# Kernel optimization log

Hardware: AMD Instinct MI355X
Metric: run time of the kernel (lower is better)

Reference implementation:

```python
import jax, jax.numpy as jnp
import numpy as np

N = 50000      # num_nodes
E = 800000     # undirected edge count (maps holds 2E directed maps)
D = 4          # stalk dimension


def setup_inputs() -> dict:
    key = jax.random.key(0)
    k1, k2, k3 = jax.random.split(key, 3)
    maps = jax.random.normal(k1, (2 * E, D, D), dtype=jnp.float32) * 0.3
    # ensure every node appears as a source at least once (avoids degenerate
    # identity eigenproblems for isolated nodes)
    row = jnp.concatenate([jnp.arange(N, dtype=jnp.int32),
                           jax.random.randint(k2, (E - N,), 0, N, dtype=jnp.int32)])
    col = jax.random.randint(k3, (E,), 0, N, dtype=jnp.int32)
    # second half of edge_index is the reversed orientation, as the module assumes
    edge_index = jnp.stack([jnp.concatenate([row, col]),
                            jnp.concatenate([col, row])])
    return {"maps": maps, "edge_index": edge_index, "num_nodes": N}


def reference(maps, edge_index, num_nodes):
    n = num_nodes
    d = maps.shape[1]
    twoE = maps.shape[0]
    Ee = twoE // 2
    row_all = edge_index[0]                                   # [2E]
    # diag contribution: R^T R per directed edge, scatter-added onto source node
    diag_contrib = jnp.einsum('eki,ekj->eij', maps, maps)     # [2E,d,d]
    maps_diag = jnp.zeros((n, d, d), maps.dtype).at[row_all].add(diag_contrib)
    row = edge_index[0, :Ee]
    col = edge_index[1, :Ee]
    # off-diagonal block: R_ij^T R_ji per undirected edge
    maps_triu = jnp.einsum('eki,ekj->eij', maps[:Ee], maps[Ee:])  # [E,d,d]
    # eval-mode augmentation: + I
    to_inv = maps_diag + jnp.eye(d, dtype=maps.dtype)
    evals, evecs = jnp.linalg.eigh(to_inv)                    # batched tiny eigh
    inv_sqrt = jnp.einsum('nik,nk,njk->nij', evecs,
                          jnp.clip(evals, 1e-8, None) ** -0.5, evecs)
    # normalize: D^{-1/2} blocks, clamp to [-1, 1]
    maps_triu = jnp.clip(jnp.einsum('eik,ekl,elj->eij',
                                    inv_sqrt[row], maps_triu, inv_sqrt[col]), -1.0, 1.0)
    maps_diag = jnp.clip(jnp.einsum('nik,nkl,nlj->nij',
                                    inv_sqrt, maps_diag, inv_sqrt), -1.0, 1.0)
    # COO assembly of the (n*d, n*d) sheaf Laplacian
    ar = jnp.arange(d, dtype=jnp.int32)
    A, B = jnp.meshgrid(ar, ar, indexing='ij')                # [d,d]
    node = jnp.arange(n, dtype=jnp.int32)
    diag_rows = (node[:, None, None] * d + A).reshape(-1)
    diag_cols = (node[:, None, None] * d + B).reshape(-1)
    tri_rows_ij = (row[:, None, None] * d + A).reshape(-1)
    tri_cols_ij = (col[:, None, None] * d + B).reshape(-1)
    tri_rows_ji = (col[:, None, None] * d + A).reshape(-1)
    tri_cols_ji = (row[:, None, None] * d + B).reshape(-1)
    rows = jnp.concatenate([diag_rows, tri_rows_ij, tri_rows_ji])
    cols = jnp.concatenate([diag_cols, tri_cols_ij, tri_cols_ji])
    vals = jnp.concatenate([maps_diag.reshape(-1),
                            (-maps_triu).reshape(-1),
                            (-jnp.swapaxes(maps_triu, 1, 2)).reshape(-1)])
    indices = jnp.stack([rows, cols])                         # [2, K]
    return indices, vals
```

## Files before the change

### kernel.cpp

```cpp
#include <hip/hip_runtime.h>

#define DEG_CAP 96

__device__ __forceinline__ void load4x4(const float* __restrict__ p, float m[4][4]) {
    const float4* q = (const float4*)p;
#pragma unroll
    for (int k = 0; k < 4; ++k) {
        float4 v = q[k];
        m[k][0] = v.x; m[k][1] = v.y; m[k][2] = v.z; m[k][3] = v.w;
    }
}

__device__ __forceinline__ void store4x4(float* __restrict__ p, const float m[4][4]) {
    float4* q = (float4*)p;
#pragma unroll
    for (int k = 0; k < 4; ++k)
        q[k] = make_float4(m[k][0], m[k][1], m[k][2], m[k][3]);
}

__device__ __forceinline__ void mmTa(const float a[4][4], const float b[4][4], float o[4][4]) {
#pragma unroll
    for (int i = 0; i < 4; ++i)
#pragma unroll
        for (int j = 0; j < 4; ++j)
            o[i][j] = a[0][i]*b[0][j] + a[1][i]*b[1][j] + a[2][i]*b[2][j] + a[3][i]*b[3][j];
}

__device__ __forceinline__ void mm(const float a[4][4], const float b[4][4], float o[4][4]) {
#pragma unroll
    for (int i = 0; i < 4; ++i)
#pragma unroll
        for (int j = 0; j < 4; ++j)
            o[i][j] = a[i][0]*b[0][j] + a[i][1]*b[1][j] + a[i][2]*b[2][j] + a[i][3]*b[3][j];
}

__global__ void k_fill(const int* __restrict__ ei, int* __restrict__ cnt,
                       int* __restrict__ bucket, int twoE) {
    int e = blockIdx.x * blockDim.x + threadIdx.x;
    if (e >= twoE) return;
    int node = ei[e];
    int slot = atomicAdd(&cnt[(size_t)node * 16], 1);
    if (slot < DEG_CAP)
        bucket[(size_t)node * DEG_CAP + slot] = e;
}

__global__ void k_gather_wave(const float* __restrict__ maps, const int* __restrict__ cnt,
                              const int* __restrict__ bucket, float* __restrict__ gram,
                              int N) {
    int tid = blockIdx.x * blockDim.x + threadIdx.x;
    int n = tid >> 6;
    int lane = threadIdx.x & 63;
    if (n >= N) return;
    int d = cnt[(size_t)n * 16];
    if (d > DEG_CAP) d = DEG_CAP;

    float G[10];
#pragma unroll
    for (int t = 0; t < 10; ++t) G[t] = 0.0f;

#pragma unroll
    for (int rep = 0; rep < 2; ++rep) {
        int slot = lane + rep * 64;
        if (slot < d) {
            int e = bucket[(size_t)n * DEG_CAP + slot];
            float m[4][4];
            load4x4(maps + (size_t)e * 16, m);
            int t = 0;
#pragma unroll
            for (int i = 0; i < 4; ++i)
#pragma unroll
                for (int j = i; j < 4; ++j, ++t)
                    G[t] += m[0][i]*m[0][j] + m[1][i]*m[1][j] + m[2][i]*m[2][j] + m[3][i]*m[3][j];
        }
    }
#pragma unroll
    for (int msk = 1; msk < 64; msk <<= 1) {
#pragma unroll
        for (int t = 0; t < 10; ++t)
            G[t] += __shfl_xor(G[t], msk, 64);
    }
    if (lane == 0) {
        float* g = gram + (size_t)n * 16;
        *(float4*)(g)     = make_float4(G[0], G[1], G[2], G[3]);
        *(float4*)(g + 4) = make_float4(G[4], G[5], G[6], G[7]);
        *(float2*)(g + 8) = make_float2(G[8], G[9]);
    }
}

__global__ void k_diag(const float* __restrict__ gram, float* __restrict__ Rtab,
                       float* __restrict__ out_vals, int N) {
    int n = blockIdx.x * blockDim.x + threadIdx.x;
    if (n >= N) return;
    const float* g = gram + (size_t)n * 16;
    float G[10];
#pragma unroll
    for (int t = 0; t < 10; ++t) G[t] = g[t];
    float D[4][4];
    {
        int t = 0;
#pragma unroll
        for (int i = 0; i < 4; ++i)
#pragma unroll
            for (int j = i; j < 4; ++j, ++t) { D[i][j] = G[t]; D[j][i] = G[t]; }
    }
    float A[4][4], V[4][4];
#pragma unroll
    for (int i = 0; i < 4; ++i)
#pragma unroll
        for (int j = 0; j < 4; ++j) {
            A[i][j] = D[i][j] + (i == j ? 1.0f : 0.0f);
            V[i][j] = (i == j) ? 1.0f : 0.0f;
        }
    const int PP[6] = {0,0,0,1,1,2};
    const int QQ[6] = {1,2,3,2,3,3};
    for (int sweep = 0; sweep < 6; ++sweep) {
        for (int r = 0; r < 6; ++r) {
            int p = PP[r], q = QQ[r];
            float apq = A[p][q];
            if (fabsf(apq) < 1e-12f) continue;
            float tau = (A[q][q] - A[p][p]) / (2.0f * apq);
            float t = copysignf(1.0f, tau) / (fabsf(tau) + sqrtf(1.0f + tau * tau));
            float c = 1.0f / sqrtf(1.0f + t * t);
            float s = t * c;
#pragma unroll
            for (int k = 0; k < 4; ++k) {
                float akp = A[k][p], akq = A[k][q];
                A[k][p] = c * akp - s * akq;
                A[k][q] = s * akp + c * akq;
            }
#pragma unroll
            for (int k = 0; k < 4; ++k) {
                float apk = A[p][k], aqk = A[q][k];
                A[p][k] = c * apk - s * aqk;
                A[q][k] = s * apk + c * aqk;
            }
#pragma unroll
            for (int k = 0; k < 4; ++k) {
                float vkp = V[k][p], vkq = V[k][q];
                V[k][p] = c * vkp - s * vkq;
                V[k][q] = s * vkp + c * vkq;
            }
        }
    }
    float w[4];
#pragma unroll
    for (int k = 0; k < 4; ++k)
        w[k] = 1.0f / sqrtf(fmaxf(A[k][k], 1e-8f));
    float R[4][4];
#pragma unroll
    for (int i = 0; i < 4; ++i)
#pragma unroll
        for (int j = 0; j < 4; ++j)
            R[i][j] = V[i][0]*w[0]*V[j][0] + V[i][1]*w[1]*V[j][1]
                    + V[i][2]*w[2]*V[j][2] + V[i][3]*w[3]*V[j][3];
    store4x4(Rtab + (size_t)n * 16, R);
    float U[4][4], O[4][4];
    mm(R, D, U);
    mm(U, R, O);
#pragma unroll
    for (int i = 0; i < 4; ++i)
#pragma unroll
        for (int j = 0; j < 4; ++j)
            O[i][j] = fminf(fmaxf(O[i][j], -1.0f), 1.0f);
    store4x4(out_vals + (size_t)n * 16, O);
}

__global__ void k_edge(const float* __restrict__ maps, const int* __restrict__ ei,
                       const float* __restrict__ Rtab,
                       float* __restrict__ out, size_t Tot, int N, int E) {
    int e = blockIdx.x * blockDim.x + threadIdx.x;
    if (e >= E) return;
    float M1[4][4], M2[4][4];
    load4x4(maps + (size_t)e * 16, M1);
    load4x4(maps + (size_t)(E + e) * 16, M2);
    int r = ei[e];
    int c = ei[2 * E + e];
    float T[4][4];
    mmTa(M1, M2, T);
    float Rr[4][4], Rc[4][4];
    load4x4(Rtab + (size_t)r * 16, Rr);
    load4x4(Rtab + (size_t)c * 16, Rc);
    float U[4][4], S[4][4];
    mm(Rr, T, U);
    mm(U, Rc, S);
#pragma unroll
    for (int i = 0; i < 4; ++i)
#pragma unroll
        for (int j = 0; j < 4; ++j)
            S[i][j] = fminf(fmaxf(S[i][j], -1.0f), 1.0f);

    float* out_rows = out;
    float* out_cols = out + Tot;
    float* out_vals = out + 2 * Tot;

    float rb = (float)(r * 4);
    float cb = (float)(c * 4);

    {
        size_t base = (size_t)16 * N + (size_t)e * 16;
        float4* qr = (float4*)(out_rows + base);
        float4* qc = (float4*)(out_cols + base);
        float4* qv = (float4*)(out_vals + base);
#pragma unroll
        for (int i = 0; i < 4; ++i) {
            float ri = rb + (float)i;
            qr[i] = make_float4(ri, ri, ri, ri);
            qc[i] = make_float4(cb, cb + 1.0f, cb + 2.0f, cb + 3.0f);
            qv[i] = make_float4(-S[i][0], -S[i][1], -S[i][2], -S[i][3]);
        }
    }
    {
        size_t base = (size_t)16 * (N + (size_t)E) + (size_t)e * 16;
        float4* qr = (float4*)(out_rows + base);
        float4* qc = (float4*)(out_cols + base);
        float4* qv = (float4*)(out_vals + base);
#pragma unroll
        for (int i = 0; i < 4; ++i) {
            float ci = cb + (float)i;
            qr[i] = make_float4(ci, ci, ci, ci);
            qc[i] = make_float4(rb, rb + 1.0f, rb + 2.0f, rb + 3.0f);
            qv[i] = make_float4(-S[0][i], -S[1][i], -S[2][i], -S[3][i]);
        }
    }
}

__global__ void k_nodeB(float* __restrict__ out, size_t Tot, int N) {
    int n = blockIdx.x * blockDim.x + threadIdx.x;
    if (n >= N) return;
    float nb = (float)(n * 4);
    float4* qr = (float4*)(out + (size_t)n * 16);
    float4* qc = (float4*)(out + Tot + (size_t)n * 16);
#pragma unroll
    for (int i = 0; i < 4; ++i) {
        float ni = nb + (float)i;
        qr[i] = make_float4(ni, ni, ni, ni);
        qc[i] = make_float4(nb, nb + 1.0f, nb + 2.0f, nb + 3.0f);
    }
}

extern "C" void kernel_launch(void* const* d_in, const int* in_sizes, int n_in,
                              void* d_out, int out_size, void* d_ws, size_t ws_size,
                              hipStream_t stream) {
    const float* maps = (const float*)d_in[0];
    const int* ei = (const int*)d_in[1];

    int twoE = in_sizes[0] / 16;
    int E = twoE / 2;
    size_t Tot = (size_t)out_size / 3;
    int N = (int)(Tot / 16) - twoE;

    float* out = (float*)d_out;
    float* out_vals = out + 2 * Tot;

    int* bucket = (int*)(out + ((size_t)out_size - (size_t)DEG_CAP * N));
    int* cnt    = (int*)(out + ((size_t)out_size - (size_t)DEG_CAP * N - (size_t)N * 16));
    float* gram =        out + ((size_t)out_size - (size_t)DEG_CAP * N - (size_t)N * 32);
    float* Rtab = out;

    hipMemsetAsync(cnt, 0, (size_t)N * 16 * sizeof(int), stream);

    int bs = 256;
    k_fill<<<(twoE + bs - 1) / bs, bs, 0, stream>>>(ei, cnt, bucket, twoE);
    k_gather_wave<<<((size_t)N * 64 + bs - 1) / bs, bs, 0, stream>>>(maps, cnt, bucket, gram, N);
    k_diag<<<(N + bs - 1) / bs, bs, 0, stream>>>(gram, Rtab, out_vals, N);
    k_edge<<<(E + bs - 1) / bs, bs, 0, stream>>>(maps, ei, Rtab, out, Tot, N, E);
    k_nodeB<<<(N + bs - 1) / bs, bs, 0, stream>>>(out, Tot, N);
}
```

Baseline: 638.0 us.

## Shard per-node atomic counters, prefetch maps in fill, use nontemporal output stores

Per-node edge counters are split into four shards chosen by the edge index, each on its own cache line, so fewer atomics contend for the same address. The fill kernel also touches the first element of each maps row to warm the cache before the gather kernel reads it. All outputs from the edge and node kernels are now written with nontemporal stores, keeping the large streaming output from evicting useful cache lines. The trade-offs are a larger counter array to clear, an extra read in fill, and a per-shard cap of 32 that can drop edges for nodes whose degree is unevenly spread across shards.

After: 949.7 us. +48.9%, slower.

```diff
diff --git a/kernel.cpp b/kernel.cpp
--- a/kernel.cpp
+++ b/kernel.cpp
@@ -1,6 +1,15 @@
 #include <hip/hip_runtime.h>
 
-#define DEG_CAP 96
+#define DEG_CAP   128
+#define NSHARD    4
+#define SHARD_CAP 32
+
+typedef float f32x4 __attribute__((ext_vector_type(4)));
+
+__device__ __forceinline__ void store_nt4(float* p, float a, float b, float c, float d) {
+    f32x4 v = {a, b, c, d};
+    __builtin_nontemporal_store(v, (f32x4*)p);
+}
 
 __device__ __forceinline__ void load4x4(const float* __restrict__ p, float m[4][4]) {
     const float4* q = (const float4*)p;
@@ -34,14 +43,17 @@
             o[i][j] = a[i][0]*b[0][j] + a[i][1]*b[1][j] + a[i][2]*b[2][j] + a[i][3]*b[3][j];
 }
 
-__global__ void k_fill(const int* __restrict__ ei, int* __restrict__ cnt,
-                       int* __restrict__ bucket, int twoE) {
+__global__ void k_fill(const int* __restrict__ ei, const float* __restrict__ maps,
+                       int* __restrict__ cnt, int* __restrict__ bucket, int twoE) {
     int e = blockIdx.x * blockDim.x + threadIdx.x;
     if (e >= twoE) return;
+    float warm = maps[(size_t)e * 16];
+    asm volatile("" :: "v"(warm));
     int node = ei[e];
-    int slot = atomicAdd(&cnt[(size_t)node * 16], 1);
-    if (slot < DEG_CAP)
-        bucket[(size_t)node * DEG_CAP + slot] = e;
+    int shard = e & (NSHARD - 1);
+    int slot = atomicAdd(&cnt[(size_t)node * 64 + shard * 16], 1);
+    if (slot < SHARD_CAP)
+        bucket[(size_t)node * DEG_CAP + shard * SHARD_CAP + slot] = e;
 }
 
 __global__ void k_gather_wave(const float* __restrict__ maps, const int* __restrict__ cnt,
@@ -51,8 +63,13 @@
     int n = tid >> 6;
     int lane = threadIdx.x & 63;
     if (n >= N) return;
-    int d = cnt[(size_t)n * 16];
-    if (d > DEG_CAP) d = DEG_CAP;
+
+    int ds[NSHARD];
+#pragma unroll
+    for (int s = 0; s < NSHARD; ++s) {
+        int c = cnt[(size_t)n * 64 + s * 16];
+        ds[s] = c > SHARD_CAP ? SHARD_CAP : c;
+    }
 
     float G[10];
 #pragma unroll
@@ -61,7 +78,9 @@
 #pragma unroll
     for (int rep = 0; rep < 2; ++rep) {
         int slot = lane + rep * 64;
-        if (slot < d) {
+        int shard = slot >> 5;
+        int idx = slot & 31;
+        if (idx < ds[shard]) {
             int e = bucket[(size_t)n * DEG_CAP + slot];
             float m[4][4];
             load4x4(maps + (size_t)e * 16, m);
@@ -198,28 +217,28 @@
 
     {
         size_t base = (size_t)16 * N + (size_t)e * 16;
-        float4* qr = (float4*)(out_rows + base);
-        float4* qc = (float4*)(out_cols + base);
-        float4* qv = (float4*)(out_vals + base);
+        float* pr = out_rows + base;
+        float* pc = out_cols + base;
+        float* pv = out_vals + base;
 #pragma unroll
         for (int i = 0; i < 4; ++i) {
             float ri = rb + (float)i;
-            qr[i] = make_float4(ri, ri, ri, ri);
-            qc[i] = make_float4(cb, cb + 1.0f, cb + 2.0f, cb + 3.0f);
-            qv[i] = make_float4(-S[i][0], -S[i][1], -S[i][2], -S[i][3]);
+            store_nt4(pr + 4 * i, ri, ri, ri, ri);
+            store_nt4(pc + 4 * i, cb, cb + 1.0f, cb + 2.0f, cb + 3.0f);
+            store_nt4(pv + 4 * i, -S[i][0], -S[i][1], -S[i][2], -S[i][3]);
         }
     }
     {
         size_t base = (size_t)16 * (N + (size_t)E) + (size_t)e * 16;
-        float4* qr = (float4*)(out_rows + base);
-        float4* qc = (float4*)(out_cols + base);
-        float4* qv = (float4*)(out_vals + base);
+        float* pr = out_rows + base;
+        float* pc = out_cols + base;
+        float* pv = out_vals + base;
 #pragma unroll
         for (int i = 0; i < 4; ++i) {
             float ci = cb + (float)i;
-            qr[i] = make_float4(ci, ci, ci, ci);
-            qc[i] = make_float4(rb, rb + 1.0f, rb + 2.0f, rb + 3.0f);
-            qv[i] = make_float4(-S[0][i], -S[1][i], -S[2][i], -S[3][i]);
+            store_nt4(pr + 4 * i, ci, ci, ci, ci);
+            store_nt4(pc + 4 * i, rb, rb + 1.0f, rb + 2.0f, rb + 3.0f);
+            store_nt4(pv + 4 * i, -S[0][i], -S[1][i], -S[2][i], -S[3][i]);
         }
     }
 }
@@ -228,13 +247,13 @@
     int n = blockIdx.x * blockDim.x + threadIdx.x;
     if (n >= N) return;
     float nb = (float)(n * 4);
-    float4* qr = (float4*)(out + (size_t)n * 16);
-    float4* qc = (float4*)(out + Tot + (size_t)n * 16);
+    float* pr = out + (size_t)n * 16;
+    float* pc = out + Tot + (size_t)n * 16;
 #pragma unroll
     for (int i = 0; i < 4; ++i) {
         float ni = nb + (float)i;
-        qr[i] = make_float4(ni, ni, ni, ni);
-        qc[i] = make_float4(nb, nb + 1.0f, nb + 2.0f, nb + 3.0f);
+        store_nt4(pr + 4 * i, ni, ni, ni, ni);
+        store_nt4(pc + 4 * i, nb, nb + 1.0f, nb + 2.0f, nb + 3.0f);
     }
 }
 
@@ -253,14 +272,14 @@
     float* out_vals = out + 2 * Tot;
 
     int* bucket = (int*)(out + ((size_t)out_size - (size_t)DEG_CAP * N));
-    int* cnt    = (int*)(out + ((size_t)out_size - (size_t)DEG_CAP * N - (size_t)N * 16));
-    float* gram =        out + ((size_t)out_size - (size_t)DEG_CAP * N - (size_t)N * 32);
+    int* cnt    = (int*)(out + ((size_t)out_size - (size_t)DEG_CAP * N - (size_t)N * 64));
+    float* gram =        out + ((size_t)out_size - (size_t)DEG_CAP * N - (size_t)N * 64 - (size_t)N * 16);
     float* Rtab = out;
 
-    hipMemsetAsync(cnt, 0, (size_t)N * 16 * sizeof(int), stream);
+    hipMemsetAsync(cnt, 0, (size_t)N * 64 * sizeof(int), stream);
 
     int bs = 256;
-    k_fill<<<(twoE + bs - 1) / bs, bs, 0, stream>>>(ei, cnt, bucket, twoE);
+    k_fill<<<(twoE + bs - 1) / bs, bs, 0, stream>>>(ei, maps, cnt, bucket, twoE);
     k_gather_wave<<<((size_t)N * 64 + bs - 1) / bs, bs, 0, stream>>>(maps, cnt, bucket, gram, N);
     k_diag<<<(N + bs - 1) / bs, bs, 0, stream>>>(gram, Rtab, out_vals, N);
     k_edge<<<(E + bs - 1) / bs, bs, 0, stream>>>(maps, ei, Rtab, out, Tot, N, E);
```
